# Kernel tuning notes

Measured on AMD Instinct MI355X. Metric: run time of the kernel, lower is better.

## Reference

```python
import jax, jax.numpy as jnp
import numpy as np

N = 100000
E = 1600000
D_IN, D_EMB, D_OUT = 16, 128, 2


def _mlp(x, W1, b1, W2, b2):
    return jax.nn.relu(x @ W1 + b1) @ W2 + b2


def _gcn(x, edge_index, edge_weight, W, b):
    # PyG GCNConv: x' = W x, symmetric norm with self-loops (weight 1), scatter-add, + bias
    n = x.shape[0]
    x = x @ W
    row, col = edge_index[0], edge_index[1]
    deg = jax.ops.segment_sum(edge_weight, col, num_segments=n) + 1.0  # +1 for self-loop
    dis = jax.lax.rsqrt(deg)
    norm = dis[row] * edge_weight * dis[col]                      # [E]
    agg = jax.ops.segment_sum(norm[:, None] * x[row], col, num_segments=n)
    agg = agg + (dis * dis)[:, None] * x                          # self-loop contribution
    return agg + b


def setup_inputs() -> dict:
    key = jax.random.key(0)
    ks = jax.random.split(key, 16)
    s_in = 1.0 / np.sqrt(D_IN)
    s_emb = 1.0 / np.sqrt(D_EMB)
    return {
        "x": jax.random.normal(ks[0], (N, D_IN), dtype=jnp.float32),
        "edge_index": jax.random.randint(ks[1], (2, E), 0, N, dtype=jnp.int64),
        "edge_weight": jax.random.uniform(ks[2], (E,), dtype=jnp.float32),
        # encoder MLP
        "enc_W1": jax.random.normal(ks[3], (D_IN, D_EMB), dtype=jnp.float32) * s_in,
        "enc_b1": jnp.zeros((D_EMB,), jnp.float32),
        "enc_W2": jax.random.normal(ks[4], (D_EMB, D_EMB), dtype=jnp.float32) * s_emb,
        "enc_b2": jnp.zeros((D_EMB,), jnp.float32),
        # conv1 / conv2
        "c1_W": jax.random.normal(ks[5], (D_EMB, D_EMB), dtype=jnp.float32) * s_emb,
        "c1_b": jnp.zeros((D_EMB,), jnp.float32),
        "c2_W": jax.random.normal(ks[6], (D_EMB, D_EMB), dtype=jnp.float32) * s_emb,
        "c2_b": jnp.zeros((D_EMB,), jnp.float32),
        # decoder MLP
        "dec_W1": jax.random.normal(ks[7], (D_EMB, D_EMB), dtype=jnp.float32) * s_emb,
        "dec_b1": jnp.zeros((D_EMB,), jnp.float32),
        "dec_W2": jax.random.normal(ks[8], (D_EMB, D_OUT), dtype=jnp.float32) * s_emb,
        "dec_b2": jnp.zeros((D_OUT,), jnp.float32),
    }


def reference(x, edge_index, edge_weight,
              enc_W1, enc_b1, enc_W2, enc_b2,
              c1_W, c1_b, c2_W, c2_b,
              dec_W1, dec_b1, dec_W2, dec_b2):
    h = _mlp(x, enc_W1, enc_b1, enc_W2, enc_b2)
    h = jax.nn.relu(_gcn(h, edge_index, edge_weight, c1_W, c1_b))
    h = jax.nn.relu(_gcn(h, edge_index, edge_weight, c2_W, c2_b))
    h = _mlp(h, dec_W1, dec_b1, dec_W2, dec_b2)
    return jax.nn.softmax(h, axis=1)
```

## Files before the change

### kernel.cpp

```cpp
#include <hip/hip_runtime.h>

#define N_NODES 100000
#define N_EDGES 1600000

typedef _Float16 half8 __attribute__((ext_vector_type(8)));
typedef float floatx4 __attribute__((ext_vector_type(4)));


__global__ __launch_bounds__(256) void edge_pass1(const int* __restrict__ ei,
                                                  const float* __restrict__ ew,
                                                  unsigned long long* __restrict__ packed,
                                                  unsigned short* __restrict__ tickets) {
    int e = blockIdx.x * 256 + threadIdx.x;
    if (e >= N_EDGES) return;
    int col = ei[N_EDGES + e];
    unsigned fx = (unsigned)(ew[e] * 1048576.0f + 0.5f);
    unsigned long long old = atomicAdd(&packed[col], (1ULL << 40) | (unsigned long long)fx);
    tickets[e] = (unsigned short)(old >> 40);
}

__global__ __launch_bounds__(256) void node_pass(const unsigned long long* __restrict__ packed,
                                                 float* __restrict__ dis,
                                                 int* __restrict__ offs,
                                                 int* __restrict__ gcur) {
    int j = blockIdx.x * 256 + threadIdx.x;
    int lane = threadIdx.x & 63;
    int c = 0;
    if (j < N_NODES) {
        unsigned long long v = packed[j];
        c = (int)(v >> 40);
        float deg = (float)(v & ((1ULL << 40) - 1)) * (1.0f / 1048576.0f);
        dis[j] = rsqrtf(deg + 1.0f);
    }
    int s = c;
    #pragma unroll
    for (int off = 1; off < 64; off <<= 1) {
        int t = __shfl_up(s, off, 64);
        if (lane >= off) s += t;
    }
    int total = __shfl(s, 63, 64);
    int base = 0;
    if (lane == 0) base = atomicAdd(gcur, total);
    base = __shfl(base, 0, 64);
    if (j < N_NODES) offs[j] = base + (s - c);
}

__global__ __launch_bounds__(256) void edge_pass2(const int* __restrict__ ei,
                                                  const float* __restrict__ ew,
                                                  const float* __restrict__ dis,
                                                  const int* __restrict__ offs,
                                                  const unsigned short* __restrict__ tickets,
                                                  unsigned* __restrict__ csr) {
    int e = blockIdx.x * 256 + threadIdx.x;
    if (e >= N_EDGES) return;
    int row = ei[e];
    int col = ei[N_EDGES + e];
    int slot = offs[col] + (int)tickets[e];
    float nw = dis[row] * ew[e] * dis[col];
    _Float16 h = (_Float16)nw;
    unsigned short hb;
    __builtin_memcpy(&hb, &h, 2);
    csr[slot] = ((unsigned)hb << 17) | (unsigned)row;
}


__global__ __launch_bounds__(256) void prep_w(const float* __restrict__ W0,
                                              const float* __restrict__ W1,
                                              const float* __restrict__ W2,
                                              const float* __restrict__ W3,
                                              _Float16* __restrict__ Wt) {
    int m = blockIdx.x >> 4;
    const float* W = (m == 0) ? W0 : (m == 1) ? W1 : (m == 2) ? W2 : W3;
    _Float16* o = Wt + m * 16384;
    int base = (blockIdx.x & 15) * 1024 + threadIdx.x * 4;
    int col = base >> 7;
    int k0 = base & 127;
    #pragma unroll
    for (int i = 0; i < 4; i++) o[base + i] = (_Float16)W[(k0 + i) * 128 + col];
}


__global__ __launch_bounds__(256) void enc1_kernel(const float* __restrict__ x,
                                                   const float* __restrict__ W1,
                                                   const float* __restrict__ b1,
                                                   _Float16* __restrict__ out) {
    __shared__ float sX[256 * 17];
    __shared__ float sW[2048];
    __shared__ float sb[128];
    int t = threadIdx.x;
    int base = blockIdx.x * 256;
    for (int i = t; i < 512; i += 256) ((float4*)sW)[i] = ((const float4*)W1)[i];
    if (t < 128) sb[t] = b1[t];
    #pragma unroll
    for (int i = 0; i < 4; i++) {
        int f = i * 1024 + t * 4;
        int row = f >> 4, k = f & 15;
        float4 v = make_float4(0.f, 0.f, 0.f, 0.f);
        if (base + row < N_NODES) v = *(const float4*)(x + (size_t)(base + row) * 16 + k);
        *(float4*)(sX + row * 17 + k) = v;
    }
    __syncthreads();
    int row = base + t;
    if (row >= N_NODES) return;
    float xr[16];
    #pragma unroll
    for (int k = 0; k < 16; k++) xr[k] = sX[t * 17 + k];
    #pragma unroll 4
    for (int cb = 0; cb < 16; cb++) {
        float acc[8];
        #pragma unroll
        for (int jj = 0; jj < 8; jj++) acc[jj] = sb[cb * 8 + jj];
        #pragma unroll
        for (int k = 0; k < 16; k++) {
            float xv = xr[k];
            #pragma unroll
            for (int jj = 0; jj < 8; jj++) acc[jj] = fmaf(xv, sW[k * 128 + cb * 8 + jj], acc[jj]);
        }
        half8 h;
        #pragma unroll
        for (int jj = 0; jj < 8; jj++) h[jj] = (_Float16)fmaxf(acc[jj], 0.f);
        *(half8*)(out + (size_t)row * 128 + cb * 8) = h;
    }
}


#define GEMM_GRID 522

template <bool BIAS, bool RELU, bool DEC>
__global__ __launch_bounds__(256, 2) void gemm_mfma(const _Float16* __restrict__ A,
                                                    const _Float16* __restrict__ Wt,
                                                    const float* __restrict__ bias,
                                                    _Float16* __restrict__ C,
                                                    const float* __restrict__ W2,
                                                    const float* __restrict__ b2,
                                                    float* __restrict__ sm_out) {
    __shared__ _Float16 sA[64 * 128];
    __shared__ _Float16 sE[DEC ? 64 : 64 * 128];
    __shared__ float sW2[DEC ? 256 : 1];
    int t = threadIdx.x;
    int lane = t & 63;
    int w = t >> 6;
    int l15 = lane & 15;
    int l4 = lane >> 4;

    half8 bfrag[8][4];
    #pragma unroll
    for (int n = 0; n < 8; n++)
        #pragma unroll
        for (int kk = 0; kk < 4; kk++)
            bfrag[n][kk] = *(const half8*)(Wt + (n * 16 + l15) * 128 + kk * 32 + l4 * 8);

    float bcol[8];
    if constexpr (BIAS) {
        #pragma unroll
        for (int n = 0; n < 8; n++) bcol[n] = bias[n * 16 + l15];
    }
    float b20 = 0.f, b21 = 0.f;
    if constexpr (DEC) {
        if (t < 256) sW2[t] = W2[t];
        b20 = b2[0]; b21 = b2[1];
    }

    const int NT = (N_NODES + 63) / 64;
    for (int tile = blockIdx.x; tile < NT; tile += GEMM_GRID) {
        const _Float16* Ag = A + (size_t)tile * 64 * 128;
        #pragma unroll
        for (int i = 0; i < 4; i++) {
            int c = i * 256 + t;
            int row = c >> 4;
            int g = (c & 15) ^ (row & 7);
            const _Float16* src = Ag + row * 128 + g * 8;
            __builtin_amdgcn_global_load_lds(
                (const __attribute__((address_space(1))) void*)src,
                (__attribute__((address_space(3))) void*)(sA + (size_t)(i * 256 + w * 64) * 8),
                16, 0, 0);
        }
        __syncthreads();

        floatx4 acc[8];
        #pragma unroll
        for (int n = 0; n < 8; n++) acc[n] = (floatx4)(0.f);

        #pragma unroll
        for (int kk = 0; kk < 4; kk++) {
            int rloc = w * 16 + l15;
            int cl = kk * 4 + l4;
            int s = cl ^ (rloc & 7);
            half8 af = *(const half8*)(sA + rloc * 128 + s * 8);
            #pragma unroll
            for (int n = 0; n < 8; n++)
                acc[n] = __builtin_amdgcn_mfma_f32_16x16x32_f16(af, bfrag[n][kk], acc[n], 0, 0, 0);
        }

        size_t base_row = (size_t)tile * 64;
        if constexpr (DEC) {
            #pragma unroll
            for (int r = 0; r < 4; r++) {
                float p0 = 0.f, p1 = 0.f;
                #pragma unroll
                for (int n = 0; n < 8; n++) {
                    float v = acc[n][r];
                    if constexpr (BIAS) v += bcol[n];
                    if constexpr (RELU) v = fmaxf(v, 0.f);
                    int ch = n * 16 + l15;
                    p0 = fmaf(v, sW2[ch * 2 + 0], p0);
                    p1 = fmaf(v, sW2[ch * 2 + 1], p1);
                }
                #pragma unroll
                for (int m = 1; m < 16; m <<= 1) {
                    p0 += __shfl_xor(p0, m, 64);
                    p1 += __shfl_xor(p1, m, 64);
                }
                size_t grow = base_row + w * 16 + l4 * 4 + r;
                if (l15 == 0 && grow < N_NODES) {
                    float z0 = p0 + b20, z1 = p1 + b21;
                    float mx = fmaxf(z0, z1);
                    float e0 = expf(z0 - mx), e1 = expf(z1 - mx);
                    float si = 1.f / (e0 + e1);
                    *(float2*)(sm_out + grow * 2) = make_float2(e0 * si, e1 * si);
                }
            }
            __syncthreads();
        } else {
            #pragma unroll
            for (int n = 0; n < 8; n++) {
                #pragma unroll
                for (int r = 0; r < 4; r++) {
                    float v = acc[n][r];
                    if constexpr (BIAS) v += bcol[n];
                    if constexpr (RELU) v = fmaxf(v, 0.f);
                    int row = w * 16 + l4 * 4 + r;
                    sE[row * 128 + n * 16 + l15] = (_Float16)v;
                }
            }
            __syncthreads();
            #pragma unroll
            for (int i = 0; i < 4; i++) {
                int c = i * 256 + t;
                int row = c >> 4;
                if (base_row + row < N_NODES) {
                    *(float4*)((char*)C + (base_row + row) * 256 + (c & 15) * 16) =
                        *(const float4*)((const char*)sE + (size_t)c * 16);
                }
            }
        }
    }
}


__device__ __forceinline__ float wdec(unsigned u) {
    unsigned short b = (unsigned short)(u >> 17);
    _Float16 h;
    __builtin_memcpy(&h, &b, 2);
    return (float)h;
}

__global__ __launch_bounds__(256) void agg_kernel(const _Float16* __restrict__ m,
                                                  const int* __restrict__ offs,
                                                  const unsigned long long* __restrict__ packed,
                                                  const unsigned* __restrict__ csr,
                                                  const float* __restrict__ dis,
                                                  const float* __restrict__ bias,
                                                  _Float16* __restrict__ out) {
    int wave = threadIdx.x >> 6;
    int lane = threadIdx.x & 63;
    int g = lane >> 4;
    int q = lane & 15;
    int j = blockIdx.x * 4 + wave;
    if (j >= N_NODES) return;
    int s = offs[j];
    int num = (int)(packed[j] >> 40);

    float acc[8];
    if (g == 0) {
        float d = dis[j];
        float dd = d * d;
        half8 mv = *(const half8*)(m + (size_t)j * 128 + q * 8);
        #pragma unroll
        for (int i = 0; i < 8; i++) acc[i] = dd * (float)mv[i];
    } else {
        #pragma unroll
        for (int i = 0; i < 8; i++) acc[i] = 0.f;
    }

    int e = 0;
    for (; e + 8 <= num; e += 8) {
        unsigned u0 = csr[s + e + g];
        unsigned u1 = csr[s + e + 4 + g];
        half8 r0 = *(const half8*)(m + (size_t)(u0 & 0x1FFFF) * 128 + q * 8);
        half8 r1 = *(const half8*)(m + (size_t)(u1 & 0x1FFFF) * 128 + q * 8);
        float w0 = wdec(u0);
        float w1 = wdec(u1);
        #pragma unroll
        for (int i = 0; i < 8; i++) acc[i] = fmaf(w0, (float)r0[i], acc[i]);
        #pragma unroll
        for (int i = 0; i < 8; i++) acc[i] = fmaf(w1, (float)r1[i], acc[i]);
    }
    for (; e < num; e += 4) {
        if (e + g < num) {
            unsigned u0 = csr[s + e + g];
            half8 r0 = *(const half8*)(m + (size_t)(u0 & 0x1FFFF) * 128 + q * 8);
            float w0 = wdec(u0);
            #pragma unroll
            for (int i = 0; i < 8; i++) acc[i] = fmaf(w0, (float)r0[i], acc[i]);
        }
    }

    #pragma unroll
    for (int i = 0; i < 8; i++) {
        acc[i] += __shfl_xor(acc[i], 16, 64);
        acc[i] += __shfl_xor(acc[i], 32, 64);
    }

    if (g == 0) {
        float4 b0 = *(const float4*)(bias + q * 8);
        float4 b1 = *(const float4*)(bias + q * 8 + 4);
        float bb[8] = {b0.x, b0.y, b0.z, b0.w, b1.x, b1.y, b1.z, b1.w};
        half8 o;
        #pragma unroll
        for (int i = 0; i < 8; i++) o[i] = (_Float16)fmaxf(acc[i] + bb[i], 0.f);
        *(half8*)(out + (size_t)j * 128 + q * 8) = o;
    }
}


extern "C" void kernel_launch(void* const* d_in, const int* in_sizes, int n_in,
                              void* d_out, int out_size, void* d_ws, size_t ws_size,
                              hipStream_t stream) {
    const float* x      = (const float*)d_in[0];
    const int*   ei     = (const int*)d_in[1];
    const float* ew     = (const float*)d_in[2];
    const float* enc_W1 = (const float*)d_in[3];
    const float* enc_b1 = (const float*)d_in[4];
    const float* enc_W2 = (const float*)d_in[5];
    const float* enc_b2 = (const float*)d_in[6];
    const float* c1_W   = (const float*)d_in[7];
    const float* c1_b   = (const float*)d_in[8];
    const float* c2_W   = (const float*)d_in[9];
    const float* c2_b   = (const float*)d_in[10];
    const float* dec_W1 = (const float*)d_in[11];
    const float* dec_b1 = (const float*)d_in[12];
    const float* dec_W2 = (const float*)d_in[13];
    const float* dec_b2 = (const float*)d_in[14];
    float* out = (float*)d_out;

    char* ws = (char*)d_ws;
    _Float16* B1 = (_Float16*)(ws);
    _Float16* B2 = (_Float16*)(ws + 25600000);
    _Float16* Wt = (_Float16*)(ws + 51200000);
    unsigned long long* packed = (unsigned long long*)(ws + 51331072);
    int*   gcur    = (int*)  (ws + 52131072);
    float* dis     = (float*)(ws + 52131328);
    int*   offs    = (int*)  (ws + 52531328);
    unsigned short* tickets = (unsigned short*)(ws + 52931328);
    unsigned* csr  = (unsigned*)(ws + 56131328);

    hipMemsetAsync(packed, 0, 800256, stream);

    edge_pass1<<<(N_EDGES + 255) / 256, 256, 0, stream>>>(ei, ew, packed, tickets);
    node_pass<<<(N_NODES + 255) / 256, 256, 0, stream>>>(packed, dis, offs, gcur);
    edge_pass2<<<(N_EDGES + 255) / 256, 256, 0, stream>>>(ei, ew, dis, offs, tickets, csr);

    prep_w<<<64, 256, 0, stream>>>(enc_W2, c1_W, c2_W, dec_W1, Wt);
    enc1_kernel<<<(N_NODES + 255) / 256, 256, 0, stream>>>(x, enc_W1, enc_b1, B1);

    gemm_mfma<true, false, false><<<GEMM_GRID, 256, 0, stream>>>(B1, Wt + 0 * 16384, enc_b2, B2, nullptr, nullptr, nullptr);
    gemm_mfma<false, false, false><<<GEMM_GRID, 256, 0, stream>>>(B2, Wt + 1 * 16384, nullptr, B1, nullptr, nullptr, nullptr);
    agg_kernel<<<N_NODES / 4, 256, 0, stream>>>(B1, offs, packed, csr, dis, c1_b, B2);
    gemm_mfma<false, false, false><<<GEMM_GRID, 256, 0, stream>>>(B2, Wt + 2 * 16384, nullptr, B1, nullptr, nullptr, nullptr);
    agg_kernel<<<N_NODES / 4, 256, 0, stream>>>(B1, offs, packed, csr, dis, c2_b, B2);
    gemm_mfma<true, true, true><<<GEMM_GRID, 256, 0, stream>>>(B2, Wt + 3 * 16384, dec_b1, nullptr, dec_W2, dec_b2, out);
}
```

Measured before the change: 452.0 us.

## Double-buffer GEMM tile loads, unroll aggregation gathers, store per-node edge counts

The MFMA GEMM now prefetches the next A tile into a second LDS buffer with async global-to-LDS loads while computing the current one, using explicit vmcnt waits and barriers instead of __syncthreads. The aggregation kernel unrolls its neighbor-gather loop from 8 to 16 edges per iteration so more row loads are in flight. It also reads a separate int count array written by node_pass instead of the 64-bit packed word. The costs are doubled LDS per block, which may reduce occupancy, more registers in the agg loop, and a hand-tuned waitcnt ordering that has to stay correct.

```diff
diff --git a/kernel.cpp b/kernel.cpp
--- a/kernel.cpp
+++ b/kernel.cpp
@@ -22,7 +22,8 @@
 __global__ __launch_bounds__(256) void node_pass(const unsigned long long* __restrict__ packed,
                                                  float* __restrict__ dis,
                                                  int* __restrict__ offs,
-                                                 int* __restrict__ gcur) {
+                                                 int* __restrict__ gcur,
+                                                 int* __restrict__ cnt) {
     int j = blockIdx.x * 256 + threadIdx.x;
     int lane = threadIdx.x & 63;
     int c = 0;
@@ -31,6 +32,7 @@
         c = (int)(v >> 40);
         float deg = (float)(v & ((1ULL << 40) - 1)) * (1.0f / 1048576.0f);
         dis[j] = rsqrtf(deg + 1.0f);
+        cnt[j] = c;
     }
     int s = c;
     #pragma unroll
@@ -134,7 +136,7 @@
                                                     const float* __restrict__ W2,
                                                     const float* __restrict__ b2,
                                                     float* __restrict__ sm_out) {
-    __shared__ _Float16 sA[64 * 128];
+    __shared__ _Float16 sA[2 * 64 * 128];
     __shared__ _Float16 sE[DEC ? 64 : 64 * 128];
     __shared__ float sW2[DEC ? 256 : 1];
     int t = threadIdx.x;
@@ -161,8 +163,7 @@
         b20 = b2[0]; b21 = b2[1];
     }
 
-    const int NT = (N_NODES + 63) / 64;
-    for (int tile = blockIdx.x; tile < NT; tile += GEMM_GRID) {
+    auto STAGE = [&](int buf, int tile) {
         const _Float16* Ag = A + (size_t)tile * 64 * 128;
         #pragma unroll
         for (int i = 0; i < 4; i++) {
@@ -172,10 +173,27 @@
             const _Float16* src = Ag + row * 128 + g * 8;
             __builtin_amdgcn_global_load_lds(
                 (const __attribute__((address_space(1))) void*)src,
-                (__attribute__((address_space(3))) void*)(sA + (size_t)(i * 256 + w * 64) * 8),
+                (__attribute__((address_space(3))) void*)(sA + buf * 8192 + (size_t)(i * 256 + w * 64) * 8),
                 16, 0, 0);
         }
-        __syncthreads();
+    };
+
+    const int NT = (N_NODES + 63) / 64;
+    int cur = 0;
+    STAGE(0, blockIdx.x);
+
+    for (int tile = blockIdx.x; tile < NT; tile += GEMM_GRID) {
+        int nx = tile + GEMM_GRID;
+        if (nx < NT) {
+            STAGE(cur ^ 1, nx);
+            asm volatile("s_waitcnt vmcnt(4)" ::: "memory");
+        } else {
+            asm volatile("s_waitcnt vmcnt(0)" ::: "memory");
+        }
+        __builtin_amdgcn_s_barrier();
+        asm volatile("" ::: "memory");
+
+        const _Float16* sAc = sA + cur * 8192;
 
         floatx4 acc[8];
         #pragma unroll
@@ -186,7 +204,7 @@
             int rloc = w * 16 + l15;
             int cl = kk * 4 + l4;
             int s = cl ^ (rloc & 7);
-            half8 af = *(const half8*)(sA + rloc * 128 + s * 8);
+            half8 af = *(const half8*)(sAc + rloc * 128 + s * 8);
             #pragma unroll
             for (int n = 0; n < 8; n++)
                 acc[n] = __builtin_amdgcn_mfma_f32_16x16x32_f16(af, bfrag[n][kk], acc[n], 0, 0, 0);
@@ -220,7 +238,8 @@
                     *(float2*)(sm_out + grow * 2) = make_float2(e0 * si, e1 * si);
                 }
             }
-            __syncthreads();
+            __builtin_amdgcn_s_barrier();
+            asm volatile("" ::: "memory");
         } else {
             #pragma unroll
             for (int n = 0; n < 8; n++) {
@@ -233,7 +252,8 @@
                     sE[row * 128 + n * 16 + l15] = (_Float16)v;
                 }
             }
-            __syncthreads();
+            __builtin_amdgcn_s_barrier();
+            asm volatile("" ::: "memory");
             #pragma unroll
             for (int i = 0; i < 4; i++) {
                 int c = i * 256 + t;
@@ -244,6 +264,7 @@
                 }
             }
         }
+        cur ^= 1;
     }
 }
 
@@ -257,7 +278,7 @@
 
 __global__ __launch_bounds__(256) void agg_kernel(const _Float16* __restrict__ m,
                                                   const int* __restrict__ offs,
-                                                  const unsigned long long* __restrict__ packed,
+                                                  const int* __restrict__ cnt,
                                                   const unsigned* __restrict__ csr,
                                                   const float* __restrict__ dis,
                                                   const float* __restrict__ bias,
@@ -269,7 +290,7 @@
     int j = blockIdx.x * 4 + wave;
     if (j >= N_NODES) return;
     int s = offs[j];
-    int num = (int)(packed[j] >> 40);
+    int num = cnt[j];
 
     float acc[8];
     if (g == 0) {
@@ -284,17 +305,24 @@
     }
 
     int e = 0;
-    for (; e + 8 <= num; e += 8) {
+    for (; e + 16 <= num; e += 16) {
         unsigned u0 = csr[s + e + g];
         unsigned u1 = csr[s + e + 4 + g];
+        unsigned u2 = csr[s + e + 8 + g];
+        unsigned u3 = csr[s + e + 12 + g];
         half8 r0 = *(const half8*)(m + (size_t)(u0 & 0x1FFFF) * 128 + q * 8);
         half8 r1 = *(const half8*)(m + (size_t)(u1 & 0x1FFFF) * 128 + q * 8);
-        float w0 = wdec(u0);
-        float w1 = wdec(u1);
+        half8 r2 = *(const half8*)(m + (size_t)(u2 & 0x1FFFF) * 128 + q * 8);
+        half8 r3 = *(const half8*)(m + (size_t)(u3 & 0x1FFFF) * 128 + q * 8);
+        float w0 = wdec(u0), w1 = wdec(u1), w2 = wdec(u2), w3 = wdec(u3);
         #pragma unroll
         for (int i = 0; i < 8; i++) acc[i] = fmaf(w0, (float)r0[i], acc[i]);
         #pragma unroll
         for (int i = 0; i < 8; i++) acc[i] = fmaf(w1, (float)r1[i], acc[i]);
+        #pragma unroll
+        for (int i = 0; i < 8; i++) acc[i] = fmaf(w2, (float)r2[i], acc[i]);
+        #pragma unroll
+        for (int i = 0; i < 8; i++) acc[i] = fmaf(w3, (float)r3[i], acc[i]);
     }
     for (; e < num; e += 4) {
         if (e + g < num) {
@@ -352,13 +380,14 @@
     int*   gcur    = (int*)  (ws + 52131072);
     float* dis     = (float*)(ws + 52131328);
     int*   offs    = (int*)  (ws + 52531328);
-    unsigned short* tickets = (unsigned short*)(ws + 52931328);
-    unsigned* csr  = (unsigned*)(ws + 56131328);
+    int*   cnt     = (int*)  (ws + 52931328);
+    unsigned short* tickets = (unsigned short*)(ws + 53331328);
+    unsigned* csr  = (unsigned*)(ws + 56531328);
 
     hipMemsetAsync(packed, 0, 800256, stream);
 
     edge_pass1<<<(N_EDGES + 255) / 256, 256, 0, stream>>>(ei, ew, packed, tickets);
-    node_pass<<<(N_NODES + 255) / 256, 256, 0, stream>>>(packed, dis, offs, gcur);
+    node_pass<<<(N_NODES + 255) / 256, 256, 0, stream>>>(packed, dis, offs, gcur, cnt);
     edge_pass2<<<(N_EDGES + 255) / 256, 256, 0, stream>>>(ei, ew, dis, offs, tickets, csr);
 
     prep_w<<<64, 256, 0, stream>>>(enc_W2, c1_W, c2_W, dec_W1, Wt);
@@ -366,8 +395,8 @@
 
     gemm_mfma<true, false, false><<<GEMM_GRID, 256, 0, stream>>>(B1, Wt + 0 * 16384, enc_b2, B2, nullptr, nullptr, nullptr);
     gemm_mfma<false, false, false><<<GEMM_GRID, 256, 0, stream>>>(B2, Wt + 1 * 16384, nullptr, B1, nullptr, nullptr, nullptr);
-    agg_kernel<<<N_NODES / 4, 256, 0, stream>>>(B1, offs, packed, csr, dis, c1_b, B2);
+    agg_kernel<<<N_NODES / 4, 256, 0, stream>>>(B1, offs, cnt, csr, dis, c1_b, B2);
     gemm_mfma<false, false, false><<<GEMM_GRID, 256, 0, stream>>>(B2, Wt + 2 * 16384, nullptr, B1, nullptr, nullptr, nullptr);
-    agg_kernel<<<N_NODES / 4, 256, 0, stream>>>(B1, offs, packed, csr, dis, c2_b, B2);
+    agg_kernel<<<N_NODES / 4, 256, 0, stream>>>(B1, offs, cnt, csr, dis, c2_b, B2);
     gemm_mfma<true, true, true><<<GEMM_GRID, 256, 0, stream>>>(B2, Wt + 3 * 16384, dec_b1, nullptr, dec_W2, dec_b2, out);
 }
```

New measurement: 448.8 us. No clear change (-0.7%).
